# Kernel optimization log

Hardware: AMD Instinct MI355X
Metric: run time of the kernel (lower is better)

## Reference

```python
import jax, jax.numpy as jnp
import numpy as np
from jax import lax

SF = 2      # scale_factor
K = 5       # up_kernel
G = 1       # up_group
CC = 64     # compressed_channels
EK = 3      # encoder_kernel


def setup_inputs() -> dict:
    key = jax.random.key(0)
    k1, k2, k3, k4, k5 = jax.random.split(key, 5)
    N, C, H, W = 4, 256, 64, 64
    x = jax.random.normal(k1, (N, C, H, W), dtype=jnp.float32)
    # channel compressor: 1x1 conv (CC, C, 1, 1), xavier-ish init
    Wc = jax.random.normal(k2, (CC, C, 1, 1), dtype=jnp.float32) * (1.0 / np.sqrt(C))
    bc = jnp.zeros((CC,), dtype=jnp.float32)
    # content encoder: 3x3 conv -> K*K*G*SF*SF channels
    enc_out = K * K * G * SF * SF
    We = jax.random.normal(k3, (enc_out, CC, EK, EK), dtype=jnp.float32) * (1.0 / np.sqrt(CC * EK * EK))
    be = jnp.zeros((enc_out,), dtype=jnp.float32)
    return {"x": x, "Wc": Wc, "bc": bc, "We": We, "be": be}


def _carafe_forward(x, Wc, bc, We, be):
    N, C, H, W = x.shape
    k2 = K * K
    # channel compressor (1x1 conv)
    comp = lax.conv_general_dilated(x, Wc, (1, 1), 'VALID') + bc[None, :, None, None]
    # content encoder (3x3 conv, padding 1)
    pad_e = (EK - 1) // 2
    m = lax.conv_general_dilated(comp, We, (1, 1), ((pad_e, pad_e), (pad_e, pad_e))) + be[None, :, None, None]
    # pixel shuffle by SF: (N, Cm*SF^2, H, W) -> (N, Cm, H*SF, W*SF)
    Cm = m.shape[1] // (SF * SF)  # == G * K*K
    m = m.reshape(N, Cm, SF, SF, H, W).transpose(0, 1, 4, 2, 5, 3).reshape(N, Cm, H * SF, W * SF)
    # softmax over kernel dimension
    m = jax.nn.softmax(m.reshape(N, G, k2, H * SF, W * SF), axis=2)
    # unfold features into kxk neighborhoods (same padding): (N, C, k2, H, W)
    pad = (K - 1) // 2
    xp = jnp.pad(x, ((0, 0), (0, 0), (pad, pad), (pad, pad)))
    patches = jnp.stack([xp[:, :, i:i + H, j:j + W] for i in range(K) for j in range(K)], axis=2)
    patches = patches.reshape(N, G, C // G, k2, H, W)
    # reassemble: contract over kernel dim BEFORE duplicating to output res.
    # out[n,g,c,h*SF+i,w*SF+j] = sum_k patches[n,g,c,k,h,w] * mask[n,g,k,h*SF+i,w*SF+j]
    mm = m.reshape(N, G, k2, H, SF, W, SF)
    out = jnp.einsum('ngckhw,ngkhiwj->ngchiwj', patches, mm)
    return out.reshape(N, C, H * SF, W * SF)


def reference(x, Wc, bc, We, be):
    return _carafe_forward(x, Wc, bc, We, be)
```

## Files before the change

### kernel.cpp

```cpp
#include <hip/hip_runtime.h>
#include <hip/hip_bf16.h>


#define COMP_F 0
#define WR_F   1115136
#define LOG_F  1179648
#define WS_NEED 11272192ull
#define CSTR 4356

__global__ void k0_wr(const float* __restrict__ We, float* __restrict__ ws) {
    int tid = blockIdx.x * blockDim.x + threadIdx.x;
    if (tid >= 4 * 5 * 64 * 45) return;
    int kk = tid % 5;
    int q  = (tid / 5) % 9;
    int cc = (tid / 45) % 64;
    int kt = (tid / 2880) % 5;
    int ij = tid / 14400;
    ws[WR_F + (size_t)(((ij * 5 + kt) * 64 + cc)) * 48 + q * 5 + kk] =
        We[(size_t)(4 * (kt * 5 + kk) + ij) * 576 + cc * 9 + q];
}

__global__ __launch_bounds__(64) void k1_comp(const float* __restrict__ x,
                                              const float* __restrict__ Wc,
                                              const float* __restrict__ bc,
                                              float* __restrict__ ws) {
    int b   = blockIdx.x;
    int pw  = b & 255;
    int ccg = b >> 8;
    int n = pw >> 6, h = pw & 63, w = threadIdx.x;
    int cc0 = ccg * 16;

    float acc[16];
#pragma unroll
    for (int u = 0; u < 16; ++u) acc[u] = 0.f;

    const float* xp = x + (size_t)n * 256 * 4096 + h * 64 + w;
#pragma unroll 8
    for (int c = 0; c < 256; ++c) {
        float xv = xp[(size_t)c * 4096];
#pragma unroll
        for (int u = 0; u < 16; ++u)
            acc[u] += xv * Wc[(cc0 + u) * 256 + c];
    }

    float* compb = ws + COMP_F + (size_t)(n * 64 + cc0) * CSTR;
#pragma unroll
    for (int u = 0; u < 16; ++u) {
        float* cb_ = compb + (size_t)u * CSTR;
        cb_[(h + 1) * 66 + (w + 1)] = acc[u] + bc[cc0 + u];
        if (w < 2) cb_[(h + 1) * 66 + (w ? 65 : 0)] = 0.f;
        if (h == 0)  { cb_[w] = 0.f;           if (w < 2) cb_[64 + w] = 0.f; }
        if (h == 63) { cb_[65 * 66 + w] = 0.f; if (w < 2) cb_[65 * 66 + 64 + w] = 0.f; }
    }
}

__global__ __launch_bounds__(256, 5) void k2_enc(const float* __restrict__ be,
                                                 float* __restrict__ ws) {
    __shared__ __align__(16) float compT[64 * 120];
    int b    = blockIdx.x;
    int tile = b & 255;
    int kt   = b >> 8;
    int n = tile >> 6, th = (tile >> 3) & 7, tw = tile & 7;
    int h0 = th * 8, w0 = tw * 8;
    int tid = threadIdx.x;

    const float* compn = ws + COMP_F + (size_t)n * 64 * CSTR;
    for (int e = tid; e < 6400; e += 256) {
        int c = e / 100, rq = e % 100, r = rq / 10, q = rq % 10;
        compT[c * 120 + r * 12 + q] =
            compn[(size_t)c * CSTR + (h0 + r) * 66 + (w0 + q)];
    }
    __syncthreads();

    int lane = tid & 63;
    int ij   = __builtin_amdgcn_readfirstlane(tid >> 6);
    int py = lane >> 3, pxx = lane & 7;

    const float* wb = ws + WR_F + (size_t)((ij * 5 + kt) * 64) * 48;

    float acc[5];
#pragma unroll
    for (int kk = 0; kk < 5; ++kk) acc[kk] = be[4 * (kt * 5 + kk) + ij];

#pragma unroll 2
    for (int c = 0; c < 64; ++c) {
        const float* cp = compT + c * 120 + py * 12 + pxx;
        float cv[9];
#pragma unroll
        for (int dy = 0; dy < 3; ++dy)
#pragma unroll
            for (int dx = 0; dx < 3; ++dx)
                cv[dy * 3 + dx] = cp[dy * 12 + dx];
        const float* w = wb + c * 48;
#pragma unroll
        for (int q = 0; q < 9; ++q) {
            float v = cv[q];
#pragma unroll
            for (int kk = 0; kk < 5; ++kk)
                acc[kk] += v * w[q * 5 + kk];
        }
    }

    float* lp = ws + LOG_F +
                (size_t)(n * 4096 + (h0 + py) * 64 + (w0 + pxx)) * 100 + ij;
#pragma unroll
    for (int kk = 0; kk < 5; ++kk) lp[4 * (kt * 5 + kk)] = acc[kk];
}

__global__ __launch_bounds__(256) void k2s_sm(float* __restrict__ ws) {
    __shared__ __align__(16) float L[64 * 100];
    float* gp = ws + LOG_F + (size_t)blockIdx.x * 6400;
    int tid = threadIdx.x;

    for (int e4 = tid; e4 < 1600; e4 += 256)
        ((float4*)L)[e4] = ((const float4*)gp)[e4];
    __syncthreads();

    int pxl = tid >> 2, ij = tid & 3;
    float* p = L + pxl * 100 + ij;
    float m[25];
#pragma unroll
    for (int k = 0; k < 25; ++k) m[k] = p[4 * k];
    float mx = m[0];
#pragma unroll
    for (int k = 1; k < 25; ++k) mx = fmaxf(mx, m[k]);
    float ss = 0.f;
#pragma unroll
    for (int k = 0; k < 25; ++k) { m[k] = __expf(m[k] - mx); ss += m[k]; }
    float inv = 1.f / ss;
#pragma unroll
    for (int k = 0; k < 25; ++k) p[4 * k] = m[k] * inv;
    __syncthreads();

    for (int e4 = tid; e4 < 1600; e4 += 256)
        ((float4*)gp)[e4] = ((const float4*)L)[e4];
}

__global__ __launch_bounds__(256) void k3_out(const float* __restrict__ x,
                                              const float* __restrict__ ws,
                                              float* __restrict__ out) {
    __shared__ __align__(16) float xt[8 * 20 * 42];
    int b      = blockIdx.x;
    int tile   = b & 63;
    int cchunk = b >> 6;
    int n = tile >> 4, ty0 = ((tile >> 2) & 3) * 16, tx0 = (tile & 3) * 16;
    int c0 = cchunk * 16;

    int py = threadIdx.x >> 4, pxx = threadIdx.x & 15;
    int h = ty0 + py, w = tx0 + pxx;

    const float* xn = x + (size_t)(n * 256 + c0) * 4096;
    for (int e2 = threadIdx.x; e2 < 3200; e2 += 256) {
        int c = e2 / 200, rem = e2 % 200, r = rem / 10, q2 = rem % 10;
        int hh = ty0 + r - 2, ww = tx0 + 2 * q2 - 2;
        float2 v = {0.f, 0.f};
        if (hh >= 0 && hh < 64 && ww >= 0 && ww < 64)
            v = *(const float2*)(xn + (size_t)c * 4096 + hh * 64 + ww);
        int a0 = (c >> 1) * 840 + r * 42 + 4 * q2 + (c & 1);
        xt[a0]     = v.x;
        xt[a0 + 2] = v.y;
    }
    __syncthreads();

    const float* lp = ws + LOG_F + (size_t)(n * 4096 + h * 64 + w) * 100;
    const float* vb = xt + py * 42 + pxx * 2;

    float2 A[8][4];
#pragma unroll
    for (int cg = 0; cg < 8; ++cg)
#pragma unroll
        for (int u = 0; u < 4; ++u) A[cg][u] = {0.f, 0.f};

    for (int dy = 0; dy < 5; ++dy) {
        const float4* mkp = (const float4*)lp + dy * 5;
        const float* vrow = vb + dy * 42;
#pragma unroll
        for (int dx = 0; dx < 5; ++dx) {
            float4 mk = mkp[dx];
#pragma unroll
            for (int cg = 0; cg < 8; ++cg) {
                float2 v = *(const float2*)(vrow + cg * 840 + dx * 2);
                A[cg][0].x += v.x * mk.x; A[cg][0].y += v.y * mk.x;
                A[cg][1].x += v.x * mk.y; A[cg][1].y += v.y * mk.y;
                A[cg][2].x += v.x * mk.z; A[cg][2].y += v.y * mk.z;
                A[cg][3].x += v.x * mk.w; A[cg][3].y += v.y * mk.w;
            }
        }
    }

#pragma unroll
    for (int cg = 0; cg < 8; ++cg) {
        int c = cg * 2;
        size_t ob0 = (((size_t)(n * 256 + c0 + c) * 128) + 2 * h) * 128 + 2 * w;
        float2 r0 = {A[cg][0].x, A[cg][1].x}, r1 = {A[cg][2].x, A[cg][3].x};
        *(float2*)(out + ob0)       = r0;
        *(float2*)(out + ob0 + 128) = r1;
        size_t ob1 = ob0 + 16384;
        float2 r2 = {A[cg][0].y, A[cg][1].y}, r3 = {A[cg][2].y, A[cg][3].y};
        *(float2*)(out + ob1)       = r2;
        *(float2*)(out + ob1 + 128) = r3;
    }
}

__global__ __launch_bounds__(256) void k_fused(const float* __restrict__ x,
                                               const float* __restrict__ Wc,
                                               const float* __restrict__ bc,
                                               const float* __restrict__ We,
                                               const float* __restrict__ be,
                                               float* __restrict__ out) {
    __shared__ float compS[64 * 101];
    int n = blockIdx.x >> 6, tile = blockIdx.x & 63;
    int ty0 = (tile >> 3) * 8, tx0 = (tile & 7) * 8;
    const float* xn = x + (size_t)n * 256 * 4096;
    {
        int pa = threadIdx.x & 127;
        int ga = __builtin_amdgcn_readfirstlane(threadIdx.x >> 7);
        bool act = pa < 100;
        int ah = ty0 + pa / 10 - 1, aw = tx0 + pa % 10 - 1;
        bool inb = act && ah >= 0 && ah < 64 && aw >= 0 && aw < 64;
        int xoff = ah * 64 + aw;
        float acc[32];
#pragma unroll
        for (int i = 0; i < 32; ++i) acc[i] = 0.f;
        for (int c = 0; c < 256; ++c) {
            float xv = inb ? xn[(size_t)c * 4096 + xoff] : 0.f;
#pragma unroll
            for (int i = 0; i < 32; ++i) acc[i] += xv * Wc[(ga * 32 + i) * 256 + c];
        }
        if (act)
#pragma unroll
            for (int i = 0; i < 32; ++i) {
                int cc = ga * 32 + i;
                compS[cc * 101 + pa] = inb ? acc[i] + bc[cc] : 0.f;
            }
    }
    __syncthreads();
    int px = threadIdx.x & 63;
    int ij = __builtin_amdgcn_readfirstlane(threadIdx.x >> 6);
    int py = px >> 3, pxx = px & 7;
    int h = ty0 + py, w = tx0 + pxx;
    float m[25];
#pragma unroll
    for (int k = 0; k < 25; ++k) m[k] = be[4 * k + ij];
    for (int cc = 0; cc < 64; ++cc) {
        float cv[9];
#pragma unroll
        for (int dy = 0; dy < 3; ++dy)
#pragma unroll
            for (int dx = 0; dx < 3; ++dx)
                cv[dy * 3 + dx] = compS[cc * 101 + (py + dy) * 10 + (pxx + dx)];
        int base = cc * 9;
#pragma unroll
        for (int k = 0; k < 25; ++k) {
            int eb = (4 * k + ij) * 576 + base;
            float s = 0.f;
#pragma unroll
            for (int qb = 0; qb < 9; ++qb) s += cv[qb] * We[eb + qb];
            m[k] += s;
        }
    }
    float mxv = m[0];
#pragma unroll
    for (int k = 1; k < 25; ++k) mxv = fmaxf(mxv, m[k]);
    float ss = 0.f;
#pragma unroll
    for (int k = 0; k < 25; ++k) { m[k] = __expf(m[k] - mxv); ss += m[k]; }
    float inv = 1.f / ss;
#pragma unroll
    for (int k = 0; k < 25; ++k) m[k] *= inv;
    int offs[25];
    unsigned vm = 0;
#pragma unroll
    for (int t = 0; t < 25; ++t) {
        int hh = h + t / 5 - 2, ww = w + t % 5 - 2;
        bool v = hh >= 0 && hh < 64 && ww >= 0 && ww < 64;
        offs[t] = v ? hh * 64 + ww : 0;
        if (v) vm |= 1u << t;
    }
    size_t outp = ((size_t)n * 256 * 128 + (2 * h + (ij >> 1))) * 128 + (2 * w + (ij & 1));
    for (int c = 0; c < 256; ++c) {
        const float* xc = xn + (size_t)c * 4096;
        float sum = 0.f;
#pragma unroll
        for (int t = 0; t < 25; ++t) {
            float v = ((vm >> t) & 1u) ? xc[offs[t]] : 0.f;
            sum += v * m[t];
        }
        out[outp + (size_t)c * 16384] = sum;
    }
}

extern "C" void kernel_launch(void* const* d_in, const int* in_sizes, int n_in,
                              void* d_out, int out_size, void* d_ws, size_t ws_size,
                              hipStream_t stream) {
    const float* x  = (const float*)d_in[0];
    const float* Wc = (const float*)d_in[1];
    const float* bc = (const float*)d_in[2];
    const float* We = (const float*)d_in[3];
    const float* be = (const float*)d_in[4];
    float* out = (float*)d_out;

    if (ws_size >= WS_NEED && d_ws != nullptr) {
        float* ws = (float*)d_ws;
        hipLaunchKernelGGL(k0_wr,   dim3(226),  dim3(256), 0, stream, We, ws);
        hipLaunchKernelGGL(k1_comp, dim3(1024), dim3(64),  0, stream, x, Wc, bc, ws);
        hipLaunchKernelGGL(k2_enc,  dim3(1280), dim3(256), 0, stream, be, ws);
        hipLaunchKernelGGL(k2s_sm,  dim3(256),  dim3(256), 0, stream, ws);
        hipLaunchKernelGGL(k3_out,  dim3(1024), dim3(256), 0, stream, x, ws, out);
    } else {
        hipLaunchKernelGGL(k_fused, dim3(256),  dim3(256), 0, stream,
                           x, Wc, bc, We, be, out);
    }
}
```

Measured before the change: 216.6 us.

## Pre-transpose Wc in workspace and retile channel compressor to 256-thread blocks

The weight-reordering kernel now also writes a transposed copy of Wc (laid out c-major, cc-minor) into the LOG_F region of the workspace. The 1x1 compressor kernel reads that copy, so each channel step loads 8 contiguous weights. It is also retiled from 64-thread blocks computing 16 output channels to 256-thread blocks computing 8 output channels over 256 pixels. The intent is better occupancy and contiguous weight loads for the compressor, at the cost of reading x twice as often (8 channel groups instead of 4). It also reuses the logits workspace region as scratch, which is only safe if the logits are written after k1 finishes.

```diff
diff --git a/kernel.cpp b/kernel.cpp
--- a/kernel.cpp
+++ b/kernel.cpp
@@ -8,44 +8,54 @@
 #define WS_NEED 11272192ull
 #define CSTR 4356
 
-__global__ void k0_wr(const float* __restrict__ We, float* __restrict__ ws) {
+__global__ void k0_wr(const float* __restrict__ We, const float* __restrict__ Wc,
+                      float* __restrict__ ws) {
     int tid = blockIdx.x * blockDim.x + threadIdx.x;
-    if (tid >= 4 * 5 * 64 * 45) return;
-    int kk = tid % 5;
-    int q  = (tid / 5) % 9;
-    int cc = (tid / 45) % 64;
-    int kt = (tid / 2880) % 5;
-    int ij = tid / 14400;
-    ws[WR_F + (size_t)(((ij * 5 + kt) * 64 + cc)) * 48 + q * 5 + kk] =
-        We[(size_t)(4 * (kt * 5 + kk) + ij) * 576 + cc * 9 + q];
-}
-
-__global__ __launch_bounds__(64) void k1_comp(const float* __restrict__ x,
-                                              const float* __restrict__ Wc,
-                                              const float* __restrict__ bc,
-                                              float* __restrict__ ws) {
-    int b   = blockIdx.x;
-    int pw  = b & 255;
-    int ccg = b >> 8;
-    int n = pw >> 6, h = pw & 63, w = threadIdx.x;
-    int cc0 = ccg * 16;
-
-    float acc[16];
-#pragma unroll
-    for (int u = 0; u < 16; ++u) acc[u] = 0.f;
-
-    const float* xp = x + (size_t)n * 256 * 4096 + h * 64 + w;
+    if (tid < 57600) {
+        int kk = tid % 5;
+        int q  = (tid / 5) % 9;
+        int cc = (tid / 45) % 64;
+        int kt = (tid / 2880) % 5;
+        int ij = tid / 14400;
+        ws[WR_F + (size_t)(((ij * 5 + kt) * 64 + cc)) * 48 + q * 5 + kk] =
+            We[(size_t)(4 * (kt * 5 + kk) + ij) * 576 + cc * 9 + q];
+    } else if (tid < 57600 + 16384) {
+        int t2 = tid - 57600;
+        int c = t2 >> 6, cc = t2 & 63;
+        ws[LOG_F + t2] = Wc[cc * 256 + c];
+    }
+}
+
+__global__ __launch_bounds__(256) void k1_comp(const float* __restrict__ x,
+                                               const float* __restrict__ bc,
+                                               float* __restrict__ ws) {
+    int b      = blockIdx.x;
+    int pxtile = b & 63;
+    int ccq    = b >> 6;
+    int tid = threadIdx.x;
+    int n   = pxtile >> 4;
+    int off = (pxtile & 15) * 256 + tid;
+    int h = off >> 6, w = off & 63;
+    int cc0 = ccq * 8;
+
+    const float* wT = ws + LOG_F;
+    const float* xp = x + (size_t)n * 256 * 4096 + off;
+
+    float acc[8];
+#pragma unroll
+    for (int u = 0; u < 8; ++u) acc[u] = 0.f;
+
 #pragma unroll 8
     for (int c = 0; c < 256; ++c) {
         float xv = xp[(size_t)c * 4096];
-#pragma unroll
-        for (int u = 0; u < 16; ++u)
-            acc[u] += xv * Wc[(cc0 + u) * 256 + c];
+        const float* wr = wT + c * 64 + cc0;
+#pragma unroll
+        for (int u = 0; u < 8; ++u) acc[u] += xv * wr[u];
     }
 
     float* compb = ws + COMP_F + (size_t)(n * 64 + cc0) * CSTR;
 #pragma unroll
-    for (int u = 0; u < 16; ++u) {
+    for (int u = 0; u < 8; ++u) {
         float* cb_ = compb + (size_t)u * CSTR;
         cb_[(h + 1) * 66 + (w + 1)] = acc[u] + bc[cc0 + u];
         if (w < 2) cb_[(h + 1) * 66 + (w ? 65 : 0)] = 0.f;
@@ -302,8 +312,8 @@
 
     if (ws_size >= WS_NEED && d_ws != nullptr) {
         float* ws = (float*)d_ws;
-        hipLaunchKernelGGL(k0_wr,   dim3(226),  dim3(256), 0, stream, We, ws);
-        hipLaunchKernelGGL(k1_comp, dim3(1024), dim3(64),  0, stream, x, Wc, bc, ws);
+        hipLaunchKernelGGL(k0_wr,   dim3(289),  dim3(256), 0, stream, We, Wc, ws);
+        hipLaunchKernelGGL(k1_comp, dim3(512),  dim3(256), 0, stream, x, bc, ws);
         hipLaunchKernelGGL(k2_enc,  dim3(1280), dim3(256), 0, stream, be, ws);
         hipLaunchKernelGGL(k2s_sm,  dim3(256),  dim3(256), 0, stream, ws);
         hipLaunchKernelGGL(k3_out,  dim3(1024), dim3(256), 0, stream, x, ws, out);
```

After: 183.9 us. -15.1%, faster.
